# Kernel tuning notes

Measured on AMD Instinct MI355X. Metric: run time of the kernel, lower is better.

The kernel has to match this reference:

```python
import jax, jax.numpy as jnp
import numpy as np

D = 1024      # embedding_dim
H = 16        # num_heads
DH = D // H   # head_dim
DFF = 4 * D
EPS = 1e-5


def setup_inputs() -> dict:
    key = jax.random.key(0)
    ks = jax.random.split(key, 10)
    B, T = 2, 2048
    s = 0.02
    return {
        "x": jax.random.normal(ks[0], (B, T, D), dtype=jnp.float32),
        "Wq": jax.random.normal(ks[1], (H, D, DH), dtype=jnp.float32) * s,
        "Wk": jax.random.normal(ks[2], (H, D, DH), dtype=jnp.float32) * s,
        "Wv": jax.random.normal(ks[3], (H, D, DH), dtype=jnp.float32) * s,
        "W1": jax.random.normal(ks[4], (D, DFF), dtype=jnp.float32) * s,
        "b1": jnp.zeros((DFF,), dtype=jnp.float32),
        "W2": jax.random.normal(ks[5], (DFF, D), dtype=jnp.float32) * s,
        "b2": jnp.zeros((D,), dtype=jnp.float32),
        "gamma1": jnp.ones((D,), dtype=jnp.float32),
        "beta1": jnp.zeros((D,), dtype=jnp.float32),
        "gamma2": jnp.ones((D,), dtype=jnp.float32),
        "beta2": jnp.zeros((D,), dtype=jnp.float32),
    }


def _layernorm(x, gamma, beta):
    # torch.var default is unbiased (ddof=1) -- faithful to LayerNorm1d
    mean = jnp.mean(x, axis=-1, keepdims=True)
    var = jnp.var(x, axis=-1, keepdims=True, ddof=1)
    return gamma * (x - mean) * jax.lax.rsqrt(var + EPS) + beta


def _block(x, Wq, Wk, Wv, W1, b1, W2, b2, gamma1, beta1, gamma2, beta2):
    B, T, _ = x.shape
    h = _layernorm(x, gamma1, beta1)
    # per-head projections stacked: [B,H,T,DH]
    Q = jnp.einsum('btd,hde->bhte', h, Wq)
    K = jnp.einsum('btd,hde->bhte', h, Wk)
    V = jnp.einsum('btd,hde->bhte', h, Wv)
    # NOTE: original scales by 1/sqrt(embedding_dim), NOT head_dim
    scores = jnp.einsum('bhqe,bhke->bhqk', Q, K) / jnp.sqrt(jnp.float32(D))
    causal = jnp.tril(jnp.ones((T, T), dtype=bool))
    scores = jnp.where(causal, scores, -jnp.inf)
    attn = jax.nn.softmax(scores, axis=-1)
    out = jnp.einsum('bhqk,bhke->bhqe', attn, V)
    # torch.cat over heads along last dim == transpose+reshape
    out = out.transpose(0, 2, 1, 3).reshape(B, T, D)
    x = x + out
    h2 = _layernorm(x, gamma2, beta2)
    ff = jax.nn.relu(h2 @ W1 + b1) @ W2 + b2  # dropout is identity at inference
    return x + ff


def reference(x, Wq, Wk, Wv, W1, b1, W2, b2, gamma1, beta1, gamma2, beta2):
    return _block(x, Wq, Wk, Wv, W1, b1, W2, b2, gamma1, beta1, gamma2, beta2)
```

## Files before the change

kernel.cpp:

```cpp
#include <hip/hip_runtime.h>

typedef unsigned short u16;
typedef __bf16 bf16;
typedef __attribute__((ext_vector_type(8))) __bf16 bf16x8;
typedef __attribute__((ext_vector_type(4))) float f32x4;
typedef __attribute__((ext_vector_type(8))) unsigned short u16x8;
typedef unsigned long long u64;

__device__ __forceinline__ float bf2f(u16 h) {
  return __uint_as_float(((unsigned int)h) << 16);
}
__device__ __forceinline__ u16 f2bf(float f) {
  unsigned int u = __float_as_uint(f);
  return (u16)((u + 0x7fffu + ((u >> 16) & 1u)) >> 16);
}
__device__ __forceinline__ u16 ld_cv(const void* p, size_t i, int f32) {
  return f32 ? f2bf(((const float*)p)[i]) : ((const u16*)p)[i];
}
__device__ __forceinline__ float ld_f(const void* p, size_t i, int f32) {
  return f32 ? ((const float*)p)[i] : bf2f(((const u16*)p)[i]);
}
__device__ __forceinline__ void async16(const u16* g, u16* l) {
  __builtin_amdgcn_global_load_lds(
      (const __attribute__((address_space(1))) unsigned int*)g,
      (__attribute__((address_space(3))) unsigned int*)l, 16, 0, 0);
}
__device__ __forceinline__ unsigned pk_bf16(float hi, float lo) {
  return __builtin_amdgcn_perm(__float_as_uint(hi) + 0x8000u,
                               __float_as_uint(lo) + 0x8000u, 0x07060302u);
}

__global__ void sniff_kernel(const u16* __restrict__ x, int* __restrict__ flag) {
  const int tid = threadIdx.x;
  int me = 0;
#pragma unroll
  for (int j = 0; j < 4; j++) {
    const u16 v = x[(tid * 4 + j) * 2];
    const int e = (v >> 7) & 0xFF;
    me = me > e ? me : e;
  }
#pragma unroll
  for (int off = 32; off > 0; off >>= 1) {
    const int o = __shfl_down(me, off);
    me = me > o ? me : o;
  }
  __shared__ int sm[4];
  if ((tid & 63) == 0) sm[tid >> 6] = me;
  __syncthreads();
  if (tid == 0) {
    int a = sm[0] > sm[1] ? sm[0] : sm[1];
    int b = sm[2] > sm[3] ? sm[2] : sm[3];
    *flag = ((a > b ? a : b) >= 140) ? 1 : 0;
  }
}

__global__ void prep_kernel(const void* __restrict__ Wq, const void* __restrict__ Wk,
                            const void* __restrict__ Wv, const void* __restrict__ W1,
                            const void* __restrict__ W2,
                            u16* __restrict__ WTq, u16* __restrict__ W1T,
                            u16* __restrict__ W2T, const int* __restrict__ flag) {
  __shared__ u16 tile[64][65];
  const int f = *flag;
  const int bid = blockIdx.x;
  const int lx = threadIdx.x & 63, ly = threadIdx.x >> 6;
  if (bid < 768) {
    const int bx = bid & 15, wh = bid >> 4;
    const int w = wh >> 4, hh = wh & 15;
    const int tr = bx * 64;
    const void* W = (w == 0) ? Wq : ((w == 1) ? Wk : Wv);
    const size_t hbase = (size_t)hh * 65536;
#pragma unroll
    for (int i = 0; i < 16; i++)
      tile[ly * 16 + i][lx] = ld_cv(W, hbase + (size_t)(tr + ly * 16 + i) * 64 + lx, f);
    __syncthreads();
#pragma unroll
    for (int i = 0; i < 16; i++)
      WTq[((size_t)(w * 1024 + hh * 64 + ly * 16 + i)) * 1024 + tr + lx] =
          tile[lx][ly * 16 + i];
  } else {
    const void* src;
    u16* dst;
    int R, C, tc, tr;
    if (bid < 1792) {
      const int j = bid - 768;
      src = W1; dst = W1T; R = 1024; C = 4096;
      tc = (j & 63) * 64; tr = (j >> 6) * 64;
    } else {
      const int j = bid - 1792;
      src = W2; dst = W2T; R = 4096; C = 1024;
      tc = (j & 15) * 64; tr = (j >> 4) * 64;
    }
#pragma unroll
    for (int i = 0; i < 16; i++)
      tile[ly * 16 + i][lx] = ld_cv(src, (size_t)(tr + ly * 16 + i) * C + tc + lx, f);
    __syncthreads();
#pragma unroll
    for (int i = 0; i < 16; i++)
      dst[(size_t)(tc + ly * 16 + i) * R + tr + lx] = tile[lx][ly * 16 + i];
  }
}

template <int EPI, int WR, int WC, bool MS>
__launch_bounds__(WR * WC * 64)
__global__ void gemm_bt(const u16* __restrict__ A, const u16* __restrict__ B,
                        int K, int NX, int N,
                        const void* __restrict__ bias, const u16* __restrict__ res,
                        void* __restrict__ out,
                        u16* __restrict__ Qo, u16* __restrict__ Ko, u16* __restrict__ Vto,
                        const int* __restrict__ flag) {
  constexpr int BM = WR * 64, BN = WC * 64, T = WR * WC * 64;
  constexpr int RPA = T / 4;
  constexpr int RAH = BM / RPA;
  constexpr int RBH = BN / RPA;
  __shared__ __align__(16) u16 As[BM * 64];
  __shared__ __align__(16) u16 Bs[BN * 64];
  const int tid = threadIdx.x;
  const int bid = blockIdx.x;
  const int sxp = NX >> 3;
  const int xcd = bid & 7, j9 = bid >> 3;
  int m0, n0;
  if (MS) {
    m0 = (xcd * sxp + j9 % sxp) * BM;
    n0 = (j9 / sxp) * BN;
  } else {
    n0 = (xcd * sxp + j9 % sxp) * BN;
    m0 = (j9 / sxp) * BM;
  }
  const int wave = tid >> 6, lane = tid & 63;
  const int wm = (wave / WC) * 64, wn = (wave % WC) * 64;
  const int lm = lane & 15, lq = lane >> 4;
  const int fb = (EPI >= 1) ? *flag : 0;

  const f32x4 zero = {0.f, 0.f, 0.f, 0.f};
  f32x4 acc[4][4];
#pragma unroll
  for (int i = 0; i < 4; i++)
#pragma unroll
    for (int j = 0; j < 4; j++) acc[i][j] = zero;

  const int ar = tid >> 2;
  const int ac = (tid & 3) * 8;
  const u16* Ag = A + (size_t)(m0 + ar) * K + ac;
  const u16* Bg = B + (size_t)(n0 + ar) * K + ac;
  u16* AsP = &As[tid * 8];
  u16* BsP = &Bs[tid * 8];

  for (int k0 = 0; k0 < K; k0 += 64) {
#pragma unroll
    for (int hh = 0; hh < 2; hh++) {
#pragma unroll
      for (int c = 0; c < RAH; c++)
        async16(Ag + k0 + hh * 32 + (size_t)c * RPA * K,
                AsP + hh * BM * 32 + c * RPA * 32);
#pragma unroll
      for (int c = 0; c < RBH; c++)
        async16(Bg + k0 + hh * 32 + (size_t)c * RPA * K,
                BsP + hh * BN * 32 + c * RPA * 32);
    }
    __syncthreads();
    bf16x8 a0[4], a1[4], b0[4], b1[4];
#pragma unroll
    for (int i = 0; i < 4; i++) {
      a0[i] = *(const bf16x8*)&As[(wm + i * 16 + lm) * 32 + lq * 8];
      a1[i] = *(const bf16x8*)&As[BM * 32 + (wm + i * 16 + lm) * 32 + lq * 8];
    }
#pragma unroll
    for (int i = 0; i < 4; i++) {
      b0[i] = *(const bf16x8*)&Bs[(wn + i * 16 + lm) * 32 + lq * 8];
      b1[i] = *(const bf16x8*)&Bs[BN * 32 + (wn + i * 16 + lm) * 32 + lq * 8];
    }
#pragma unroll
    for (int i = 0; i < 4; i++)
#pragma unroll
      for (int j = 0; j < 4; j++) {
        acc[i][j] = __builtin_amdgcn_mfma_f32_16x16x32_bf16(a0[i], b0[j], acc[i][j], 0, 0, 0);
        acc[i][j] = __builtin_amdgcn_mfma_f32_16x16x32_bf16(a1[i], b1[j], acc[i][j], 0, 0, 0);
      }
    __syncthreads();
  }

  if (EPI == 0) {
#pragma unroll
    for (int i = 0; i < 4; i++) {
      const int row0 = m0 + wm + i * 16 + lq * 4;
      const int bb = row0 >> 11, t0 = row0 & 2047;
#pragma unroll
      for (int j = 0; j < 4; j++) {
        const int col = n0 + wn + j * 16 + lm;
        const int w = col >> 10, nn = col & 1023;
        const int hh = nn >> 6, e = nn & 63;
        if (w == 2) {
          ushort4 v4;
          v4.x = f2bf(acc[i][j][0]);
          v4.y = f2bf(acc[i][j][1]);
          v4.z = f2bf(acc[i][j][2]);
          v4.w = f2bf(acc[i][j][3]);
          *(ushort4*)&Vto[(((size_t)(bb * 16 + hh)) * 64 + e) * 2048 + t0] = v4;
        } else {
          u16* dst = (w == 0) ? Qo : Ko;
#pragma unroll
          for (int r = 0; r < 4; r++)
            dst[(((size_t)(bb * 16 + hh)) * 2048 + t0 + r) * 64 + e] =
                f2bf(acc[i][j][r]);
        }
      }
    }
  } else {
#pragma unroll
    for (int i = 0; i < 4; i++) {
#pragma unroll
      for (int r = 0; r < 4; r++) {
        const int row = m0 + wm + i * 16 + lq * 4 + r;
#pragma unroll
        for (int j = 0; j < 4; j++) {
          const int col = n0 + wn + j * 16 + lm;
          const float c = acc[i][j][r];
          if (EPI == 1) {
            const float v = c + ld_f(bias, col, fb);
            ((u16*)out)[(size_t)row * N + col] = f2bf(v > 0.f ? v : 0.f);
          } else {
            const float v = c + ld_f(bias, col, fb) + bf2f(res[(size_t)row * N + col]);
            if (fb)
              ((float*)out)[(size_t)row * N + col] = v;
            else
              ((u16*)out)[(size_t)row * N + col] = f2bf(v);
          }
        }
      }
    }
  }
}

__launch_bounds__(256)
__global__ void attn_mfma(const u16* __restrict__ Q, const u16* __restrict__ K,
                          const u16* __restrict__ Vt, const void* __restrict__ xres,
                          const int* __restrict__ flag, u16* __restrict__ x2) {
  __shared__ __align__(16) unsigned char smem[35328];
  const int tid = threadIdx.x;
  const int wave = tid >> 6, lane = tid & 63;
  const int lm = lane & 15, quad = lane >> 4;
  const int bid = blockIdx.x;
  const int xcd = bid & 7, jj = bid >> 3;
  const int bh = xcd + 8 * (jj & 3);
  const int pair = jj >> 2;
  const int b = bh >> 4, h = bh & 15;
  const int f32in = *flag;

  u16* stw = (u16*)smem + wave * 4096;
  u16* Ksw = stw;
  u16* Vsw = stw + 2048;
  float (*Olds)[32][68] = (float(*)[32][68])smem;
  float (*Llds)[2][16] = (float(*)[2][16])(smem + 34816);

  const u16* Kbh = K + (size_t)bh * 131072;
  const u16* Vbh = Vt + (size_t)bh * 131072;
  const f32x4 zero = {0.f, 0.f, 0.f, 0.f};
  const int srow = lane >> 2;
  const int schk = (lane & 3) * 8;

  union V8 { bf16x8 v; struct { u64 lo, hi; } q; };

#pragma unroll 1
  for (int phase = 0; phase < 2; phase++) {
    const int qb = phase ? (63 - pair) : pair;
    const int qw0 = qb * 32;

    bf16x8 qf[2][2];
#pragma unroll
    for (int s = 0; s < 2; s++) {
      const u16* Qp = Q + ((size_t)bh * 2048 + qw0 + s * 16 + lm) * 64 + quad * 8;
      qf[s][0] = *(const bf16x8*)Qp;
      qf[s][1] = *(const bf16x8*)(Qp + 32);
    }
    f32x4 ot[2][4];
#pragma unroll
    for (int s = 0; s < 2; s++)
#pragma unroll
      for (int j = 0; j < 4; j++) ot[s][j] = zero;
    float l[2] = {0.f, 0.f};

    const int nt = qb + 1;
    const int si = (nt * wave) >> 2;
    const int ei = (nt * (wave + 1)) >> 2;

    for (int t = si; t < ei; t++) {
      const int ks = t * 32;
#pragma unroll
      for (int hh2 = 0; hh2 < 2; hh2++)
#pragma unroll
        for (int c = 0; c < 2; c++)
          async16(Kbh + (size_t)(ks + c * 16 + srow) * 64 + hh2 * 32 + schk,
                  Ksw + hh2 * 1024 + c * 512 + lane * 8);
#pragma unroll
      for (int c = 0; c < 4; c++)
        async16(Vbh + (size_t)(c * 16 + srow) * 2048 + ks + schk,
                Vsw + c * 512 + lane * 8);
      __builtin_amdgcn_s_waitcnt(0x0F70);

      f32x4 S[2][2];
#pragma unroll
      for (int s = 0; s < 2; s++)
#pragma unroll
        for (int hh = 0; hh < 2; hh++) {
          const bf16x8 k0 = *(const bf16x8*)&Ksw[(hh * 16 + lm) * 32 + quad * 8];
          const bf16x8 k1 = *(const bf16x8*)&Ksw[1024 + (hh * 16 + lm) * 32 + quad * 8];
          f32x4 a = zero;
          a = __builtin_amdgcn_mfma_f32_16x16x32_bf16(k0, qf[s][0], a, 0, 0, 0);
          a = __builtin_amdgcn_mfma_f32_16x16x32_bf16(k1, qf[s][1], a, 0, 0, 0);
          S[s][hh] = a;
        }
      const bool maskT = (t == qb);
#pragma unroll
      for (int s = 0; s < 2; s++) {
        float p[2][4];
#pragma unroll
        for (int hh = 0; hh < 2; hh++)
#pragma unroll
          for (int r = 0; r < 4; r++) {
            float v = __expf(S[s][hh][r] * 0.03125f);
            if (maskT && (hh * 16 + quad * 4 + r > s * 16 + lm)) v = 0.f;
            l[s] += v;
            p[hh][r] = v;
          }
        unsigned pk[4];
        pk[0] = pk_bf16(p[0][1], p[0][0]);
        pk[1] = pk_bf16(p[0][3], p[0][2]);
        pk[2] = pk_bf16(p[1][1], p[1][0]);
        pk[3] = pk_bf16(p[1][3], p[1][2]);
        const bf16x8 pf = *(const bf16x8*)pk;
#pragma unroll
        for (int j = 0; j < 4; j++) {
          V8 vf;
          vf.q.lo = *(const u64*)&Vsw[(j * 16 + lm) * 32 + quad * 4];
          vf.q.hi = *(const u64*)&Vsw[(j * 16 + lm) * 32 + 16 + quad * 4];
          ot[s][j] = __builtin_amdgcn_mfma_f32_16x16x32_bf16(vf.v, pf, ot[s][j], 0, 0, 0);
        }
      }
    }

#pragma unroll
    for (int s = 0; s < 2; s++) {
      l[s] += __shfl_xor(l[s], 16);
      l[s] += __shfl_xor(l[s], 32);
    }

    __syncthreads();

#pragma unroll
    for (int s = 0; s < 2; s++)
#pragma unroll
      for (int j = 0; j < 4; j++)
        *(f32x4*)&Olds[wave][s * 16 + lm][j * 16 + quad * 4] = ot[s][j];
    if (quad == 0) {
      Llds[wave][0][lm] = l[0];
      Llds[wave][1][lm] = l[1];
    }
    __syncthreads();
    const int q = tid >> 3;
    const int e0 = (tid & 7) * 8;
    f32x4 oa = zero, ob = zero;
#pragma unroll
    for (int w = 0; w < 4; w++) {
      oa += *(const f32x4*)&Olds[w][q][e0];
      ob += *(const f32x4*)&Olds[w][q][e0 + 4];
    }
    const float lt = Llds[0][q >> 4][q & 15] + Llds[1][q >> 4][q & 15] +
                     Llds[2][q >> 4][q & 15] + Llds[3][q >> 4][q & 15];
    const float linv = 1.f / lt;
    const size_t rowbase = ((size_t)(b * 2048 + qw0 + q)) * 1024 + h * 64 + e0;
    float xv[8];
    if (f32in) {
      const float* xf = (const float*)xres + rowbase;
      const float4 u0 = *(const float4*)xf;
      const float4 u1 = *(const float4*)(xf + 4);
      xv[0] = u0.x; xv[1] = u0.y; xv[2] = u0.z; xv[3] = u0.w;
      xv[4] = u1.x; xv[5] = u1.y; xv[6] = u1.z; xv[7] = u1.w;
    } else {
      const u16x8 u = *(const u16x8*)((const u16*)xres + rowbase);
#pragma unroll
      for (int k = 0; k < 8; k++) xv[k] = bf2f(u[k]);
    }
    u16x8 o8;
#pragma unroll
    for (int k = 0; k < 4; k++) o8[k] = f2bf(xv[k] + oa[k] * linv);
#pragma unroll
    for (int k = 0; k < 4; k++) o8[4 + k] = f2bf(xv[4 + k] + ob[k] * linv);
    *(u16x8*)&x2[rowbase] = o8;
    __syncthreads();
  }
}

__launch_bounds__(256)
__global__ void ln_kernel(const void* __restrict__ x, const void* __restrict__ gamma,
                          const void* __restrict__ beta, u16* __restrict__ out,
                          const int* __restrict__ flag, int xraw) {
  const size_t row = blockIdx.x;
  const int tid = threadIdx.x;
  const int f = *flag;
  const int fx = xraw ? f : 0;
  float v0, v1, v2, v3;
  if (fx) {
    const float4 v = *((const float4*)x + row * 256 + tid);
    v0 = v.x; v1 = v.y; v2 = v.z; v3 = v.w;
  } else {
    const ushort4 u = *((const ushort4*)x + row * 256 + tid);
    v0 = bf2f(u.x); v1 = bf2f(u.y); v2 = bf2f(u.z); v3 = bf2f(u.w);
  }
  float s = v0 + v1 + v2 + v3;
  float sq = v0 * v0 + v1 * v1 + v2 * v2 + v3 * v3;
#pragma unroll
  for (int off = 32; off > 0; off >>= 1) {
    s += __shfl_down(s, off);
    sq += __shfl_down(sq, off);
  }
  __shared__ float ss[4], ssq[4];
  if ((tid & 63) == 0) { ss[tid >> 6] = s; ssq[tid >> 6] = sq; }
  __syncthreads();
  s = ss[0] + ss[1] + ss[2] + ss[3];
  sq = ssq[0] + ssq[1] + ssq[2] + ssq[3];
  const float mean = s * (1.f / 1024.f);
  const float var = (sq - 1024.f * mean * mean) * (1.f / 1023.f);
  const float rs = rsqrtf(var + 1e-5f);
  const int c0 = tid * 4;
  ushort4 o;
  o.x = f2bf(ld_f(gamma, c0 + 0, f) * (v0 - mean) * rs + ld_f(beta, c0 + 0, f));
  o.y = f2bf(ld_f(gamma, c0 + 1, f) * (v1 - mean) * rs + ld_f(beta, c0 + 1, f));
  o.z = f2bf(ld_f(gamma, c0 + 2, f) * (v2 - mean) * rs + ld_f(beta, c0 + 2, f));
  o.w = f2bf(ld_f(gamma, c0 + 3, f) * (v3 - mean) * rs + ld_f(beta, c0 + 3, f));
  *(ushort4*)&out[row * 1024 + tid * 4] = o;
}

extern "C" void kernel_launch(void* const* d_in, const int* in_sizes, int n_in,
                              void* d_out, int out_size, void* d_ws, size_t ws_size,
                              hipStream_t stream) {
  const void* x      = d_in[0];
  const void* Wq     = d_in[1];
  const void* Wk     = d_in[2];
  const void* Wv     = d_in[3];
  const void* W1     = d_in[4];
  const void* b1     = d_in[5];
  const void* W2     = d_in[6];
  const void* b2     = d_in[7];
  const void* gamma1 = d_in[8];
  const void* beta1  = d_in[9];
  const void* gamma2 = d_in[10];
  const void* beta2  = d_in[11];
  u16* ws = (u16*)d_ws;

  const size_t M4 = 4194304;
  u16* h   = ws;
  u16* Qb  = ws + 1 * M4;
  u16* Kb  = ws + 2 * M4;
  u16* Vtb = ws + 3 * M4;
  u16* WTq = ws + 4 * M4;
  u16* x2  = ws + 4 * M4;
  u16* h2  = ws + 5 * M4;
  u16* W1T = ws + 6 * M4;
  u16* W2T = ws + 7 * M4;
  u16* ff1 = ws;
  int* flag = (int*)(ws + 8 * M4 + 9216);

  sniff_kernel<<<1, 256, 0, stream>>>((const u16*)x, flag);
  prep_kernel<<<2816, 256, 0, stream>>>(Wq, Wk, Wv, W1, W2, WTq, W1T, W2T, flag);
  ln_kernel<<<4096, 256, 0, stream>>>(x, gamma1, beta1, h, flag, 1);
  gemm_bt<0, 2, 2, false><<<768, 256, 0, stream>>>(h, WTq, 1024, 24, 3072,
                                                   nullptr, nullptr, nullptr,
                                                   Qb, Kb, Vtb, flag);
  attn_mfma<<<1024, 256, 0, stream>>>(Qb, Kb, Vtb, x, flag, x2);
  ln_kernel<<<4096, 256, 0, stream>>>(x2, gamma2, beta2, h2, flag, 0);
  gemm_bt<1, 2, 2, false><<<1024, 256, 0, stream>>>(h2, W1T, 1024, 32, 4096,
                                                    b1, nullptr, ff1,
                                                    nullptr, nullptr, nullptr, flag);
  gemm_bt<2, 2, 1, true><<<512, 128, 0, stream>>>(ff1, W2T, 4096, 32, 1024,
                                                  b2, x2, d_out,
                                                  nullptr, nullptr, nullptr, flag);
}
```

Before: 374.9 us.

## Add intra-block split-K GEMM for FFN down-projection and enlarge other GEMM tiles

```diff
diff --git a/kernel.cpp b/kernel.cpp
--- a/kernel.cpp
+++ b/kernel.cpp
@@ -232,6 +232,98 @@
 }
 
 __launch_bounds__(256)
+__global__ void gemm_sk(const u16* __restrict__ A, const u16* __restrict__ B,
+                        const void* __restrict__ bias, const u16* __restrict__ res,
+                        void* __restrict__ out, const int* __restrict__ flag) {
+  __shared__ __align__(16) unsigned char smem[33536];
+  u16* As = (u16*)smem;
+  u16* Bs = (u16*)smem + 8192;
+  float* Ml = (float*)smem;
+  const int tid = threadIdx.x;
+  const int bid = blockIdx.x;
+  const int xcd = bid & 7, j9 = bid >> 3;
+  const int m0 = (xcd * 4 + j9 % 4) * 128;
+  const int n0 = (j9 / 4) * 64;
+  const int wave = tid >> 6, lane = tid & 63;
+  const int wm = (wave & 1) * 64, kh = wave >> 1;
+  const int lm = lane & 15, lq = lane >> 4;
+  const int fb = *flag;
+
+  const f32x4 zero = {0.f, 0.f, 0.f, 0.f};
+  f32x4 acc[4][4];
+#pragma unroll
+  for (int i = 0; i < 4; i++)
+#pragma unroll
+    for (int j = 0; j < 4; j++) acc[i][j] = zero;
+
+  const int ar = tid >> 2;
+  const int ac = (tid & 3) * 8;
+  const u16* Ag = A + (size_t)(m0 + ar) * 4096 + ac;
+  const u16* Bg = B + (size_t)(n0 + ar) * 4096 + ac;
+  const int khash = kh * 4096;
+  const int khbs = kh * 2048;
+
+  for (int k0 = 0; k0 < 2048; k0 += 32) {
+#pragma unroll
+    for (int khh = 0; khh < 2; khh++) {
+#pragma unroll
+      for (int c = 0; c < 2; c++)
+        async16(Ag + khh * 2048 + k0 + (size_t)c * 64 * 4096,
+                As + khh * 4096 + c * 2048 + tid * 8);
+      async16(Bg + khh * 2048 + k0, Bs + khh * 2048 + tid * 8);
+    }
+    __syncthreads();
+    bf16x8 a[4], b[4];
+#pragma unroll
+    for (int i = 0; i < 4; i++)
+      a[i] = *(const bf16x8*)&As[khash + (wm + i * 16 + lm) * 32 + lq * 8];
+#pragma unroll
+    for (int j = 0; j < 4; j++)
+      b[j] = *(const bf16x8*)&Bs[khbs + (j * 16 + lm) * 32 + lq * 8];
+#pragma unroll
+    for (int i = 0; i < 4; i++)
+#pragma unroll
+      for (int j = 0; j < 4; j++)
+        acc[i][j] = __builtin_amdgcn_mfma_f32_16x16x32_bf16(a[i], b[j], acc[i][j], 0, 0, 0);
+    __syncthreads();
+  }
+
+  __syncthreads();
+  if (kh == 1) {
+    const int mh = wave & 1;
+#pragma unroll
+    for (int i = 0; i < 4; i++)
+#pragma unroll
+      for (int j = 0; j < 4; j++)
+#pragma unroll
+        for (int r = 0; r < 4; r++)
+          Ml[mh * 4160 + (i * 16 + lq * 4 + r) * 65 + j * 16 + lm] = acc[i][j][r];
+  }
+  __syncthreads();
+  if (kh == 0) {
+    const int mh = wave & 1;
+#pragma unroll
+    for (int i = 0; i < 4; i++) {
+#pragma unroll
+      for (int r = 0; r < 4; r++) {
+        const int row = m0 + wm + i * 16 + lq * 4 + r;
+#pragma unroll
+        for (int j = 0; j < 4; j++) {
+          const int col = n0 + j * 16 + lm;
+          const float c = acc[i][j][r] +
+                          Ml[mh * 4160 + (i * 16 + lq * 4 + r) * 65 + j * 16 + lm];
+          const float v = c + ld_f(bias, col, fb) + bf2f(res[(size_t)row * 1024 + col]);
+          if (fb)
+            ((float*)out)[(size_t)row * 1024 + col] = v;
+          else
+            ((u16*)out)[(size_t)row * 1024 + col] = f2bf(v);
+        }
+      }
+    }
+  }
+}
+
+__launch_bounds__(256)
 __global__ void attn_mfma(const u16* __restrict__ Q, const u16* __restrict__ K,
                           const u16* __restrict__ Vt, const void* __restrict__ xres,
                           const int* __restrict__ flag, u16* __restrict__ x2) {
@@ -463,15 +555,13 @@
   sniff_kernel<<<1, 256, 0, stream>>>((const u16*)x, flag);
   prep_kernel<<<2816, 256, 0, stream>>>(Wq, Wk, Wv, W1, W2, WTq, W1T, W2T, flag);
   ln_kernel<<<4096, 256, 0, stream>>>(x, gamma1, beta1, h, flag, 1);
-  gemm_bt<0, 2, 2, false><<<768, 256, 0, stream>>>(h, WTq, 1024, 24, 3072,
+  gemm_bt<0, 4, 2, false><<<384, 512, 0, stream>>>(h, WTq, 1024, 24, 3072,
                                                    nullptr, nullptr, nullptr,
                                                    Qb, Kb, Vtb, flag);
   attn_mfma<<<1024, 256, 0, stream>>>(Qb, Kb, Vtb, x, flag, x2);
   ln_kernel<<<4096, 256, 0, stream>>>(x2, gamma2, beta2, h2, flag, 0);
-  gemm_bt<1, 2, 2, false><<<1024, 256, 0, stream>>>(h2, W1T, 1024, 32, 4096,
-                                                    b1, nullptr, ff1,
-                                                    nullptr, nullptr, nullptr, flag);
-  gemm_bt<2, 2, 1, true><<<512, 128, 0, stream>>>(ff1, W2T, 4096, 32, 1024,
-                                                  b2, x2, d_out,
-                                                  nullptr, nullptr, nullptr, flag);
-}
+  gemm_bt<1, 4, 2, false><<<512, 512, 0, stream>>>(h2, W1T, 1024, 32, 4096,
+                                                   b1, nullptr, ff1,
+                                                   nullptr, nullptr, nullptr, flag);
+  gemm_sk<<<512, 256, 0, stream>>>(ff1, W2T, b2, x2, d_out, flag);
+}
```

Result: faster. 350.8 us (-6.4%).
